# Performance work log

Measured on AMD Instinct MI355X. Metric: run time of the kernel, lower is better.

The kernel has to match this reference:

```python
import jax, jax.numpy as jnp
import numpy as np

N = 100000      # nodes
E = 1600000     # edges
G = 100         # graphs in batch
D_IN, H, OUT = 3, 128, 10


def gcn_conv(x, W, b, src, dst, n_nodes):
    """PyG GCNConv with default add_self_loops=True, symmetric normalization.
    out_i = sum_{j->i} d_j^-1/2 d_i^-1/2 (x_j W) + d_i^-1 (x_i W) + b
    where d includes the self-loop (+1)."""
    h = x @ W                                                   # [N, F]
    ones = jnp.ones((src.shape[0],), dtype=x.dtype)
    deg = jax.ops.segment_sum(ones, dst, num_segments=n_nodes) + 1.0  # self-loop
    dinv_sqrt = jax.lax.rsqrt(deg)
    norm = dinv_sqrt[src] * dinv_sqrt[dst]                      # [E]
    msg = h[src] * norm[:, None]                                # gather + scale
    agg = jax.ops.segment_sum(msg, dst, num_segments=n_nodes)   # scatter-add
    out = agg + h * (1.0 / deg)[:, None] + b                    # self-loop term + bias
    return out


def setup_inputs() -> dict:
    key = jax.random.key(0)
    ks = jax.random.split(key, 9)
    x = jax.random.normal(ks[0], (N, D_IN), dtype=jnp.float32)
    edge_index = jax.random.randint(ks[1], (2, E), 0, N)
    batch = jnp.sort(jax.random.randint(ks[2], (N,), 0, G))
    W1 = jax.random.normal(ks[3], (D_IN, H), dtype=jnp.float32) * (1.0 / np.sqrt(D_IN))
    b1 = jnp.zeros((H,), dtype=jnp.float32)
    W2 = jax.random.normal(ks[4], (H, H), dtype=jnp.float32) * (1.0 / np.sqrt(H))
    b2 = jnp.zeros((H,), dtype=jnp.float32)
    Wl = jax.random.normal(ks[5], (H, OUT), dtype=jnp.float32) * (1.0 / np.sqrt(H))
    bl = jnp.zeros((OUT,), dtype=jnp.float32)
    return {"x": x, "edge_index": edge_index, "batch": batch,
            "W1": W1, "b1": b1, "W2": W2, "b2": b2, "Wl": Wl, "bl": bl}


def reference(x, edge_index, batch, W1, b1, W2, b2, Wl, bl):
    src, dst = edge_index[0], edge_index[1]
    h = jax.nn.relu(gcn_conv(x, W1, b1, src, dst, N))
    h = jax.nn.relu(gcn_conv(h, W2, b2, src, dst, N))
    # global mean pool over graphs
    sums = jax.ops.segment_sum(h, batch, num_segments=G)                 # [G, H]
    cnts = jax.ops.segment_sum(jnp.ones((N,), h.dtype), batch, num_segments=G)
    pooled = sums / jnp.maximum(cnts, 1.0)[:, None]
    # dropout p=0.5 is identity in eval mode
    return pooled @ Wl + bl                                              # [G, OUT]
```

## Files before the change

kernel.cpp:

```cpp
#include <hip/hip_runtime.h>


#define DIN 3
#define H 128
#define OUTF 10
#define NWEIGHT (384 + 128 + 16384 + 128 + 1280 + 10)
#define ECH 2048
#define RGSH 9
#define RGSIZE 512
#define W2FRAG_N 16384
#define CHE 512

typedef float gcn364_f2 __attribute__((ext_vector_type(2)));
typedef float gcn364_f4 __attribute__((ext_vector_type(4)));
typedef short gcn364_s8 __attribute__((ext_vector_type(8)));

__device__ __forceinline__ float gcn364_bf2f(unsigned short u) {
    return __uint_as_float(((unsigned int)u) << 16);
}
__device__ __forceinline__ unsigned short gcn364_f2bf(float f) {
    unsigned int u = __float_as_uint(f);
    u += 0x7FFFu + ((u >> 16) & 1u);
    return (unsigned short)(u >> 16);
}

__device__ __forceinline__ int gcn364_probe(const unsigned short* __restrict__ xs16) {
    int lane = threadIdx.x & 63;
    int outl = 0;
    #pragma unroll
    for (int k = 0; k < 4; k++) {
        unsigned short u = xs16[lane * 4 + k];
        int e = (u >> 7) & 0xFF;
        outl += (e < 100 || e > 140) ? 1 : 0;
    }
    #pragma unroll
    for (int d = 1; d < 64; d <<= 1) outl += __shfl_xor(outl, d);
    return (outl > 32) ? 1 : 0;
}

static __global__ void gcn364_histconv(const void* __restrict__ x,
                                       const void* __restrict__ W1, const void* __restrict__ b1,
                                       const void* __restrict__ W2, const void* __restrict__ b2,
                                       const void* __restrict__ Wl, const void* __restrict__ bl,
                                       int* __restrict__ flag,
                                       float4* __restrict__ xf4, float* __restrict__ wf,
                                       unsigned short* __restrict__ w2frag,
                                       float* __restrict__ pooled,
                                       const int* __restrict__ edst,
                                       int* __restrict__ hist,
                                       int N, int E, int S, int RG, int GH) {
    __shared__ int h[256];
    if (blockIdx.x < (unsigned)S) {
        h[threadIdx.x] = 0;
        __syncthreads();
        int elo = blockIdx.x * ECH;
        int ehi = elo + ECH; if (ehi > E) ehi = E;
        #pragma unroll 4
        for (int e = elo + threadIdx.x; e < ehi; e += 256)
            atomicAdd(&h[edst[e] >> RGSH], 1);
        __syncthreads();
        if (threadIdx.x < RG) hist[blockIdx.x * RG + threadIdx.x] = h[threadIdx.x];
    }
    int i = blockIdx.x * blockDim.x + threadIdx.x;
    if (i < GH) pooled[i] = 0.0f;
    int total = N + NWEIGHT;
    if ((int)blockIdx.x * 256 < total) {
        int fl = gcn364_probe((const unsigned short*)x);
        if (i == 0) *flag = fl;
        if (i < N) {
            float a, b, c;
            if (fl) {
                const float* xs = (const float*)x;
                a = xs[3 * i]; b = xs[3 * i + 1]; c = xs[3 * i + 2];
            } else {
                const unsigned short* xs = (const unsigned short*)x;
                a = gcn364_bf2f(xs[3 * i]);
                b = gcn364_bf2f(xs[3 * i + 1]);
                c = gcn364_bf2f(xs[3 * i + 2]);
            }
            xf4[i] = make_float4(a, b, c, 0.f);
        } else if (i < total) {
            int j = i - N;
            const void* srcp;
            if      (j < 384)                       { srcp = W1; }
            else if ((j -= 384)   < 128)            { srcp = b1; }
            else if ((j -= 128)   < 16384)          { srcp = W2; }
            else if ((j -= 16384) < 128)            { srcp = b2; }
            else if ((j -= 128)   < 1280)           { srcp = Wl; }
            else    { j -= 1280;                      srcp = bl; }
            wf[i - N] = fl ? ((const float*)srcp)[j]
                           : gcn364_bf2f(((const unsigned short*)srcp)[j]);
        }
        if (i < W2FRAG_N) {
            int fl2 = fl;
            int j = i & 7;
            int l = (i >> 3) & 63;
            int c = (i >> 9) & 3;
            int t = i >> 11;
            int k = c * 32 + (l >> 4) * 8 + j;
            int n = t * 16 + (l & 15);
            float w = fl2 ? ((const float*)W2)[k * H + n]
                          : gcn364_bf2f(((const unsigned short*)W2)[k * H + n]);
            w2frag[i] = gcn364_f2bf(w);
        }
    }
}

static __global__ void gcn364_scanHpar(int* __restrict__ hist,
                                       int* __restrict__ regionBase,
                                       int S, int RG) {
    __shared__ int sh[1024];
    int r = blockIdx.x;
    int t = threadIdx.x;
    int carry = 0;
    for (int s0 = 0; s0 < S; s0 += 1024) {
        int s = s0 + t;
        int c = (s < S) ? hist[s * RG + r] : 0;
        sh[t] = c;
        __syncthreads();
        for (int d = 1; d < 1024; d <<= 1) {
            int v = (t >= d) ? sh[t - d] : 0;
            __syncthreads();
            sh[t] += v;
            __syncthreads();
        }
        if (s < S) hist[s * RG + r] = carry + sh[t] - c;
        int tot = sh[1023];
        __syncthreads();
        carry += tot;
    }
    if (t == 0) regionBase[r] = carry;
}

static __global__ void gcn364_scanR(int* __restrict__ regionBase,
                                    int RG, int E) {
    __shared__ int sh[256];
    int t = threadIdx.x;
    int c = (t < RG) ? regionBase[t] : 0;
    sh[t] = c;
    __syncthreads();
    for (int d = 1; d < 256; d <<= 1) {
        int v = (t >= d) ? sh[t - d] : 0;
        __syncthreads();
        sh[t] += v;
        __syncthreads();
    }
    if (t < RG) regionBase[t] = sh[t] - c;
    if (t == 0) regionBase[RG] = E;
}

static __global__ void gcn364_partition(const int* __restrict__ src,
                                        const int* __restrict__ dst,
                                        const int* __restrict__ hist,
                                        const int* __restrict__ regionBase,
                                        int* __restrict__ epack,
                                        int E, int RG) {
    __shared__ int gbase[256];
    __shared__ int scnt[256];
    __shared__ int sbase[256];
    __shared__ int ebuf[ECH];
    __shared__ unsigned char rmap[ECH];
    int s = blockIdx.x;
    int t = threadIdx.x;
    int elo = s * ECH;
    int ehi = elo + ECH; if (ehi > E) ehi = E;
    int ne = ehi - elo;

    if (t < RG) gbase[t] = hist[s * RG + t] + regionBase[t];
    scnt[t] = 0;
    __syncthreads();
    #pragma unroll 4
    for (int e = elo + t; e < ehi; e += 256)
        atomicAdd(&scnt[dst[e] >> RGSH], 1);
    __syncthreads();
    int c = scnt[t];
    sbase[t] = c;
    __syncthreads();
    for (int d = 1; d < 256; d <<= 1) {
        int v = (t >= d) ? sbase[t - d] : 0;
        __syncthreads();
        sbase[t] += v;
        __syncthreads();
    }
    int excl = sbase[t] - c;
    __syncthreads();
    sbase[t] = excl;
    scnt[t] = 0;
    __syncthreads();
    #pragma unroll 4
    for (int e = elo + t; e < ehi; e += 256) {
        int d = dst[e];
        int r = d >> RGSH;
        int lofs = atomicAdd(&scnt[r], 1);
        int slot = sbase[r] + lofs;
        ebuf[slot] = ((d & (RGSIZE - 1)) << 17) | src[e];
        rmap[slot] = (unsigned char)r;
    }
    __syncthreads();
    #pragma unroll 4
    for (int k = t; k < ne; k += 256) {
        int r = rmap[k];
        epack[gbase[r] + (k - sbase[r])] = ebuf[k];
    }
}

static __global__ void gcn364_build(const int* __restrict__ epack,
                                    const int* __restrict__ regionBase,
                                    int* __restrict__ off,
                                    int* __restrict__ esrc,
                                    float4* __restrict__ xf4,
                                    int N) {
    __shared__ int sdeg[RGSIZE];
    __shared__ int stmp[256];
    int r = blockIdx.x;
    int nlo = r << RGSH;
    int nn = N - nlo; if (nn > RGSIZE) nn = RGSIZE;
    int e0 = regionBase[r];
    int e1 = regionBase[r + 1];
    int t = threadIdx.x;
    int bdim = blockDim.x;

    if (t < RGSIZE) sdeg[t] = 0;
    __syncthreads();
    #pragma unroll 4
    for (int p = e0 + t; p < e1; p += bdim)
        atomicAdd(&sdeg[epack[p] >> 17], 1);
    __syncthreads();

    int a0 = 0, a1 = 0, psum = 0;
    if (t < 256) {
        a0 = sdeg[2 * t];
        a1 = sdeg[2 * t + 1];
        psum = a0 + a1;
        stmp[t] = psum;
    }
    __syncthreads();
    for (int d = 1; d < 256; d <<= 1) {
        int val = (t >= d && t < 256) ? stmp[t - d] : 0;
        __syncthreads();
        if (t < 256) stmp[t] += val;
        __syncthreads();
    }
    if (t < 256) {
        int excl = stmp[t] - psum;

        if (2 * t < nn)     off[nlo + 2 * t]     = e0 + excl + a0;
        if (2 * t + 1 < nn) off[nlo + 2 * t + 1] = e0 + excl + a0 + a1;
        if (2 * t < nn) {
            float di = rsqrtf((float)a0 + 1.0f);
            float4 xv = xf4[nlo + 2 * t];
            xv.x *= di; xv.y *= di; xv.z *= di; xv.w = di;
            xf4[nlo + 2 * t] = xv;
        }
        if (2 * t + 1 < nn) {
            float di = rsqrtf((float)a1 + 1.0f);
            float4 xv = xf4[nlo + 2 * t + 1];
            xv.x *= di; xv.y *= di; xv.z *= di; xv.w = di;
            xf4[nlo + 2 * t + 1] = xv;
        }
        sdeg[2 * t]     = e0 + excl;
        sdeg[2 * t + 1] = e0 + excl + a0;
    }
    __syncthreads();
    #pragma unroll 4
    for (int p = e0 + t; p < e1; p += bdim) {
        int v = epack[p];
        int q = atomicAdd(&sdeg[v >> 17], 1);
        esrc[q] = v & 0x1FFFF;
    }
}

static __global__ void gcn364_aggu(const int* __restrict__ esrc,
                                   const int* __restrict__ off,
                                   const float4* __restrict__ xf4,
                                   float4* __restrict__ u4, int N) {
    int lane = threadIdx.x & 63;
    int wv = threadIdx.x >> 6;
    int grp = lane >> 4;
    int sub = lane & 15;
    int i = (blockIdx.x * 4 + wv) * 4 + grp;

    float a0 = 0.f, a1 = 0.f, a2 = 0.f;
    if (i < N) {
        int p0 = (i == 0) ? 0 : off[i - 1];
        int p1 = off[i];
        for (int p = p0 + sub; p < p1; p += 16) {
            float4 sv = xf4[esrc[p]];
            a0 += sv.x; a1 += sv.y; a2 += sv.z;
        }
    }
    for (int d = 1; d < 16; d <<= 1) {
        a0 += __shfl_xor(a0, d);
        a1 += __shfl_xor(a1, d);
        a2 += __shfl_xor(a2, d);
    }
    if (i < N && sub == 0) {
        float4 xi = xf4[i];
        float di = xi.w;
        u4[i] = make_float4(di * (a0 + xi.x), di * (a1 + xi.y), di * (a2 + xi.z), di);
    }
}

__device__ __forceinline__ void gcn364_edge(const float4 u,
                                            const gcn364_f2* wa2, const gcn364_f2* wb2,
                                            const gcn364_f2* wc2, const gcn364_f2* bb2,
                                            gcn364_f2* acc) {
    gcn364_f2 ux = {u.x, u.x}, uy = {u.y, u.y}, uz = {u.z, u.z}, uw = {u.w, u.w};
    gcn364_f2 zero = {0.f, 0.f};
    #pragma unroll
    for (int q = 0; q < 4; q++) {
        gcn364_f2 t = ux * wa2[q] + uy * wb2[q] + uz * wc2[q] + bb2[q];
        t = __builtin_elementwise_max(t, zero);
        acc[q] += uw * t;
    }
}

#define MPB 16
static __global__ __launch_bounds__(256, 8) void gcn364_agg2pool(
        const int* __restrict__ esrc, const int* __restrict__ off,
        const float4* __restrict__ u4,
        const float* __restrict__ w1f, const float* __restrict__ b1f,
        const unsigned short* __restrict__ w2frag, const float* __restrict__ b2f,
        const int* __restrict__ batch, float* __restrict__ pooled, int N) {
    __shared__ unsigned short vshb[MPB][H + 8];
    __shared__ float4 sstage[CHE];
    __shared__ int soff[MPB + 1];
    __shared__ int sbatch[MPB];
    __shared__ float spool[2][H];
    int i0 = blockIdx.x * MPB;
    int tid = threadIdx.x;
    int wave = tid >> 6;
    int lane = tid & 63;
    int grp = lane >> 4;
    int sub = lane & 15;
    int node = wave * 4 + grp;
    int i = i0 + node;

    if (tid <= MPB) {
        int idx = i0 - 1 + tid;
        int cidx = idx < N - 1 ? idx : N - 1;
        soff[tid] = (idx < 0) ? 0 : off[cidx];
    }
    if (tid < MPB) {
        int bi = i0 + tid; if (bi > N - 1) bi = N - 1;
        sbatch[tid] = batch[bi];
    }

    gcn364_f2 wa2[4], wb2[4], wc2[4], bb2[4];
    #pragma unroll
    for (int q = 0; q < 4; q++) {
        int f = sub * 8 + q * 2;
        wa2[q] = (gcn364_f2){w1f[f], w1f[f + 1]};
        wb2[q] = (gcn364_f2){w1f[H + f], w1f[H + f + 1]};
        wc2[q] = (gcn364_f2){w1f[2 * H + f], w1f[2 * H + f + 1]};
        bb2[q] = (gcn364_f2){b1f[f], b1f[f + 1]};
    }
    __syncthreads();

    int s  = soff[node];
    int e  = soff[node + 1];
    int e0 = soff[0];
    int e1 = soff[MPB];

    gcn364_f2 acc[4];
    acc[0] = acc[1] = acc[2] = acc[3] = (gcn364_f2){0.f, 0.f};
    for (int cb = e0; cb < e1; cb += CHE) {
        int ce = cb + CHE; if (ce > e1) ce = e1;
        for (int p = cb + tid; p < ce; p += 256)
            sstage[p - cb] = u4[esrc[p]];
        __syncthreads();
        int lo = s > cb ? s : cb;
        int hi = e < ce ? e : ce;
        #pragma unroll 4
        for (int p = lo; p < hi; p++) {
            float4 u = sstage[p - cb];
            gcn364_edge(u, wa2, wb2, wc2, bb2, acc);
        }
        __syncthreads();
    }
    float di = 0.f;
    if (i < N) {
        float4 uS = u4[i];
        gcn364_edge(uS, wa2, wb2, wc2, bb2, acc);
        di = uS.w;
    }
    {
        gcn364_s8 o;
        o[0] = (short)gcn364_f2bf(acc[0].x * di);
        o[1] = (short)gcn364_f2bf(acc[0].y * di);
        o[2] = (short)gcn364_f2bf(acc[1].x * di);
        o[3] = (short)gcn364_f2bf(acc[1].y * di);
        o[4] = (short)gcn364_f2bf(acc[2].x * di);
        o[5] = (short)gcn364_f2bf(acc[2].y * di);
        o[6] = (short)gcn364_f2bf(acc[3].x * di);
        o[7] = (short)gcn364_f2bf(acc[3].y * di);
        *(gcn364_s8*)&vshb[node][sub * 8] = o;
    }
    __syncthreads();

    int m = lane & 15;
    int quad = lane >> 4;
    int g0 = sbatch[0];
    gcn364_s8 af[4];
    #pragma unroll
    for (int c = 0; c < 4; c++)
        af[c] = *(const gcn364_s8*)&vshb[m][c * 32 + quad * 8];

    #pragma unroll
    for (int tt = 0; tt < 2; tt++) {
        int t = wave * 2 + tt;
        gcn364_f4 cacc = {0.f, 0.f, 0.f, 0.f};
        #pragma unroll
        for (int c = 0; c < 4; c++) {
            gcn364_s8 bf8 = *(const gcn364_s8*)&w2frag[(((t * 4 + c) * 64) + lane) * 8];
            cacc = __builtin_amdgcn_mfma_f32_16x16x32_bf16(af[c], bf8, cacc, 0, 0, 0);
        }
        int feat = t * 16 + m;
        float bb = b2f[feat];
        int baseRow = quad * 4;
        float sum0 = 0.0f, sum1 = 0.0f;
        #pragma unroll
        for (int r = 0; r < 4; r++) {
            int ii = i0 + baseRow + r;
            if (ii >= N) continue;
            float val = fmaxf(cacc[r] + bb, 0.0f);
            if (sbatch[baseRow + r] == g0) sum0 += val; else sum1 += val;
        }
        sum0 += __shfl_xor(sum0, 16); sum0 += __shfl_xor(sum0, 32);
        sum1 += __shfl_xor(sum1, 16); sum1 += __shfl_xor(sum1, 32);
        if (quad == 0) {
            spool[0][feat] = sum0;
            spool[1][feat] = sum1;
        }
    }
    __syncthreads();
    {
        int slot = tid >> 7;
        int f = tid & (H - 1);
        float v = spool[slot][f];
        if (v != 0.0f) {
            int g = slot ? sbatch[MPB - 1] : g0;
            atomicAdd(&pooled[g * H + f], v);
        }
    }
}

static __global__ void gcn364_final(const float* __restrict__ pooled,
                                    const int* __restrict__ batch,
                                    const float* __restrict__ wlf,
                                    const float* __restrict__ blf,
                                    const int* __restrict__ flag,
                                    void* __restrict__ out, int N, int G) {
    int g = blockIdx.x;
    int o = threadIdx.x;
    if (g >= G || o >= OUTF) return;
    int lo = 0, hi = N;
    while (lo < hi) { int m = (lo + hi) >> 1; if (batch[m] < g) lo = m + 1; else hi = m; }
    int a = lo;
    lo = 0; hi = N;
    while (lo < hi) { int m = (lo + hi) >> 1; if (batch[m] < g + 1) lo = m + 1; else hi = m; }
    float cn = (float)(lo - a);
    float inv = 1.0f / fmaxf(cn, 1.0f);
    float acc = 0.0f;
    for (int k = 0; k < H; k++)
        acc += pooled[g * H + k] * wlf[k * OUTF + o];
    float v = acc * inv + blf[o];
    if (*flag) ((float*)out)[g * OUTF + o] = v;
    else       ((unsigned short*)out)[g * OUTF + o] = gcn364_f2bf(v);
}

extern "C" void kernel_launch(void* const* d_in, const int* in_sizes, int n_in,
                              void* d_out, int out_size, void* d_ws, size_t ws_size,
                              hipStream_t stream) {
    const void* x  = d_in[0];
    const int* edge_index = (const int*)d_in[1];
    const int* batch      = (const int*)d_in[2];
    const void* W1 = d_in[3];
    const void* b1 = d_in[4];
    const void* W2 = d_in[5];
    const void* b2 = d_in[6];
    const void* Wl = d_in[7];
    const void* bl = d_in[8];

    const int N = in_sizes[0] / DIN;
    const int E = in_sizes[1] / 2;
    const int G = out_size / OUTF;
    const int* src = edge_index;
    const int* dst = edge_index + E;
    const int SH = (E + 8191) / 8192;
    const int S  = (E + ECH - 1) / ECH;
    const int RG = (N + RGSIZE - 1) >> RGSH;
    const int GH = G * H;

    char* wsb = (char*)d_ws;
    float* pooled     = (float*)wsb;
    int*   histLeg    = (int*)(pooled + (size_t)GH);
    int*   regionBase = histLeg + (size_t)SH * RG;
    int*   off        = regionBase + RG + 1;
    int*   flag       = off + N;
    size_t ofs = (((size_t)((char*)(flag + 1) - wsb)) + 15) & ~(size_t)15;
    float4* xf4  = (float4*)(wsb + ofs);
    float4* u4   = xf4 + N;
    float*  wf   = (float*)(u4 + N);
    size_t ofs2 = (((size_t)((char*)(wf + NWEIGHT) - wsb)) + 15) & ~(size_t)15;
    unsigned short* w2frag = (unsigned short*)(wsb + ofs2);
    int*    epack = (int*)(w2frag + W2FRAG_N);
    int*    esrc  = epack + E;
    int*    hist  = esrc;

    float* w1f = wf;
    float* b1f = w1f + 384;
    float* b2f = b1f + 128 + 16384;
    float* wlf = b2f + 128;
    float* blf = wlf + 1280;

    {
        int convBlocks = (N + NWEIGHT + 255) / 256;
        int gmax = (S > convBlocks) ? S : convBlocks;
        gcn364_histconv<<<gmax, 256, 0, stream>>>(
            x, W1, b1, W2, b2, Wl, bl, flag, xf4, wf, w2frag, pooled,
            dst, hist, N, E, S, RG, GH);
    }
    gcn364_scanHpar<<<RG, 1024, 0, stream>>>(hist, regionBase, S, RG);
    gcn364_scanR<<<1, 256, 0, stream>>>(regionBase, RG, E);
    gcn364_partition<<<S, 256, 0, stream>>>(src, dst, hist, regionBase, epack, E, RG);
    gcn364_build<<<RG, 1024, 0, stream>>>(epack, regionBase, off, esrc, xf4, N);
    gcn364_aggu<<<(N + 15) / 16, 256, 0, stream>>>(esrc, off, xf4, u4, N);
    gcn364_agg2pool<<<(N + MPB - 1) / MPB, 256, 0, stream>>>(
        esrc, off, u4, w1f, b1f, w2frag, b2f, batch, pooled, N);
    gcn364_final<<<G, 64, 0, stream>>>(pooled, batch, wlf, blf, flag, d_out, N, G);
}
```

Before: 182.8 us.

## Vectorize edge loads, reuse scanned histogram in partition, parallelize final projection

The histogram and partition kernels now read dst/src as int4 when the chunk is aligned. The partition kernel drops its own counting pass and derives per-chunk region counts from the already-scanned histogram. The final kernel uses 128 threads with a wave shuffle reduction instead of a serial 128-step dot product per output. The layer-1 weight loads in agg2pool are also vectorized. Together these cut a full re-read of dst and some serial latency, at the cost of alignment-checked dual code paths and a dependence on the hist layout written by scanHpar.

Result: faster. 177.6 us (-2.8%).

```diff
diff --git a/kernel.cpp b/kernel.cpp
--- a/kernel.cpp
+++ b/kernel.cpp
@@ -55,9 +55,23 @@
         __syncthreads();
         int elo = blockIdx.x * ECH;
         int ehi = elo + ECH; if (ehi > E) ehi = E;
-        #pragma unroll 4
-        for (int e = elo + threadIdx.x; e < ehi; e += 256)
-            atomicAdd(&h[edst[e] >> RGSH], 1);
+        int ne = ehi - elo;
+        if (((ne & 3) == 0) && ((((size_t)(edst + elo)) & 15) == 0)) {
+            const int4* d4 = (const int4*)(edst + elo);
+            int n4 = ne >> 2;
+            #pragma unroll 2
+            for (int k = threadIdx.x; k < n4; k += 256) {
+                int4 v = d4[k];
+                atomicAdd(&h[v.x >> RGSH], 1);
+                atomicAdd(&h[v.y >> RGSH], 1);
+                atomicAdd(&h[v.z >> RGSH], 1);
+                atomicAdd(&h[v.w >> RGSH], 1);
+            }
+        } else {
+            #pragma unroll 4
+            for (int e = elo + threadIdx.x; e < ehi; e += 256)
+                atomicAdd(&h[edst[e] >> RGSH], 1);
+        }
         __syncthreads();
         if (threadIdx.x < RG) hist[blockIdx.x * RG + threadIdx.x] = h[threadIdx.x];
     }
@@ -154,7 +168,7 @@
                                         const int* __restrict__ hist,
                                         const int* __restrict__ regionBase,
                                         int* __restrict__ epack,
-                                        int E, int RG) {
+                                        int E, int S, int RG) {
     __shared__ int gbase[256];
     __shared__ int scnt[256];
     __shared__ int sbase[256];
@@ -166,15 +180,15 @@
     int ehi = elo + ECH; if (ehi > E) ehi = E;
     int ne = ehi - elo;
 
-    if (t < RG) gbase[t] = hist[s * RG + t] + regionBase[t];
+    int cnt = 0;
+    if (t < RG) {
+        int own = hist[s * RG + t];
+        gbase[t] = own + regionBase[t];
+        if (s < S - 1) cnt = hist[(s + 1) * RG + t] - own;
+        else           cnt = (regionBase[t + 1] - regionBase[t]) - own;
+    }
     scnt[t] = 0;
-    __syncthreads();
-    #pragma unroll 4
-    for (int e = elo + t; e < ehi; e += 256)
-        atomicAdd(&scnt[dst[e] >> RGSH], 1);
-    __syncthreads();
-    int c = scnt[t];
-    sbase[t] = c;
+    sbase[t] = cnt;
     __syncthreads();
     for (int d = 1; d < 256; d <<= 1) {
         int v = (t >= d) ? sbase[t - d] : 0;
@@ -182,19 +196,40 @@
         sbase[t] += v;
         __syncthreads();
     }
-    int excl = sbase[t] - c;
+    int excl = sbase[t] - cnt;
     __syncthreads();
     sbase[t] = excl;
-    scnt[t] = 0;
-    __syncthreads();
-    #pragma unroll 4
-    for (int e = elo + t; e < ehi; e += 256) {
-        int d = dst[e];
-        int r = d >> RGSH;
-        int lofs = atomicAdd(&scnt[r], 1);
-        int slot = sbase[r] + lofs;
-        ebuf[slot] = ((d & (RGSIZE - 1)) << 17) | src[e];
-        rmap[slot] = (unsigned char)r;
+    __syncthreads();
+    if (((ne & 3) == 0) && ((((size_t)(dst + elo)) & 15) == 0) &&
+        ((((size_t)(src + elo)) & 15) == 0)) {
+        const int4* d4 = (const int4*)(dst + elo);
+        const int4* s4 = (const int4*)(src + elo);
+        int n4 = ne >> 2;
+        #pragma unroll 2
+        for (int k = t; k < n4; k += 256) {
+            int4 dv = d4[k];
+            int4 sv = s4[k];
+            int r0 = dv.x >> RGSH, r1 = dv.y >> RGSH;
+            int r2 = dv.z >> RGSH, r3 = dv.w >> RGSH;
+            int p0 = sbase[r0] + atomicAdd(&scnt[r0], 1);
+            ebuf[p0] = ((dv.x & (RGSIZE - 1)) << 17) | sv.x; rmap[p0] = (unsigned char)r0;
+            int p1 = sbase[r1] + atomicAdd(&scnt[r1], 1);
+            ebuf[p1] = ((dv.y & (RGSIZE - 1)) << 17) | sv.y; rmap[p1] = (unsigned char)r1;
+            int p2 = sbase[r2] + atomicAdd(&scnt[r2], 1);
+            ebuf[p2] = ((dv.z & (RGSIZE - 1)) << 17) | sv.z; rmap[p2] = (unsigned char)r2;
+            int p3 = sbase[r3] + atomicAdd(&scnt[r3], 1);
+            ebuf[p3] = ((dv.w & (RGSIZE - 1)) << 17) | sv.w; rmap[p3] = (unsigned char)r3;
+        }
+    } else {
+        #pragma unroll 4
+        for (int e = elo + t; e < ehi; e += 256) {
+            int d = dst[e];
+            int r = d >> RGSH;
+            int lofs = atomicAdd(&scnt[r], 1);
+            int slot = sbase[r] + lofs;
+            ebuf[slot] = ((d & (RGSIZE - 1)) << 17) | src[e];
+            rmap[slot] = (unsigned char)r;
+        }
     }
     __syncthreads();
     #pragma unroll 4
@@ -347,13 +382,23 @@
     }
 
     gcn364_f2 wa2[4], wb2[4], wc2[4], bb2[4];
-    #pragma unroll
-    for (int q = 0; q < 4; q++) {
-        int f = sub * 8 + q * 2;
-        wa2[q] = (gcn364_f2){w1f[f], w1f[f + 1]};
-        wb2[q] = (gcn364_f2){w1f[H + f], w1f[H + f + 1]};
-        wc2[q] = (gcn364_f2){w1f[2 * H + f], w1f[2 * H + f + 1]};
-        bb2[q] = (gcn364_f2){b1f[f], b1f[f + 1]};
+    {
+        const gcn364_f4* wA = (const gcn364_f4*)w1f;
+        const gcn364_f4* wB = (const gcn364_f4*)(w1f + H);
+        const gcn364_f4* wC = (const gcn364_f4*)(w1f + 2 * H);
+        const gcn364_f4* wD = (const gcn364_f4*)b1f;
+        gcn364_f4 a0 = wA[sub * 2], a1 = wA[sub * 2 + 1];
+        gcn364_f4 b0 = wB[sub * 2], b1v = wB[sub * 2 + 1];
+        gcn364_f4 c0 = wC[sub * 2], c1 = wC[sub * 2 + 1];
+        gcn364_f4 d0 = wD[sub * 2], d1 = wD[sub * 2 + 1];
+        wa2[0] = (gcn364_f2){a0[0], a0[1]}; wa2[1] = (gcn364_f2){a0[2], a0[3]};
+        wa2[2] = (gcn364_f2){a1[0], a1[1]}; wa2[3] = (gcn364_f2){a1[2], a1[3]};
+        wb2[0] = (gcn364_f2){b0[0], b0[1]}; wb2[1] = (gcn364_f2){b0[2], b0[3]};
+        wb2[2] = (gcn364_f2){b1v[0], b1v[1]}; wb2[3] = (gcn364_f2){b1v[2], b1v[3]};
+        wc2[0] = (gcn364_f2){c0[0], c0[1]}; wc2[1] = (gcn364_f2){c0[2], c0[3]};
+        wc2[2] = (gcn364_f2){c1[0], c1[1]}; wc2[3] = (gcn364_f2){c1[2], c1[3]};
+        bb2[0] = (gcn364_f2){d0[0], d0[1]}; bb2[1] = (gcn364_f2){d0[2], d0[3]};
+        bb2[2] = (gcn364_f2){d1[0], d1[1]}; bb2[3] = (gcn364_f2){d1[2], d1[3]};
     }
     __syncthreads();
 
@@ -451,9 +496,12 @@
                                     const float* __restrict__ blf,
                                     const int* __restrict__ flag,
                                     void* __restrict__ out, int N, int G) {
+    __shared__ float red[2][OUTF];
     int g = blockIdx.x;
-    int o = threadIdx.x;
-    if (g >= G || o >= OUTF) return;
+    int t = threadIdx.x;
+    int lane = t & 63;
+    int wv = t >> 6;
+    if (g >= G) return;
     int lo = 0, hi = N;
     while (lo < hi) { int m = (lo + hi) >> 1; if (batch[m] < g) lo = m + 1; else hi = m; }
     int a = lo;
@@ -461,12 +509,26 @@
     while (lo < hi) { int m = (lo + hi) >> 1; if (batch[m] < g + 1) lo = m + 1; else hi = m; }
     float cn = (float)(lo - a);
     float inv = 1.0f / fmaxf(cn, 1.0f);
-    float acc = 0.0f;
-    for (int k = 0; k < H; k++)
-        acc += pooled[g * H + k] * wlf[k * OUTF + o];
-    float v = acc * inv + blf[o];
-    if (*flag) ((float*)out)[g * OUTF + o] = v;
-    else       ((unsigned short*)out)[g * OUTF + o] = gcn364_f2bf(v);
+
+    float p = pooled[g * H + t];
+    float v[OUTF];
+    #pragma unroll
+    for (int o = 0; o < OUTF; o++) v[o] = p * wlf[t * OUTF + o];
+    #pragma unroll
+    for (int d = 1; d < 64; d <<= 1) {
+        #pragma unroll
+        for (int o = 0; o < OUTF; o++) v[o] += __shfl_xor(v[o], d);
+    }
+    if (lane == 0) {
+        #pragma unroll
+        for (int o = 0; o < OUTF; o++) red[wv][o] = v[o];
+    }
+    __syncthreads();
+    if (t < OUTF) {
+        float r = (red[0][t] + red[1][t]) * inv + blf[t];
+        if (*flag) ((float*)out)[g * OUTF + t] = r;
+        else       ((unsigned short*)out)[g * OUTF + t] = gcn364_f2bf(r);
+    }
 }
 
 extern "C" void kernel_launch(void* const* d_in, const int* in_sizes, int n_in,
@@ -523,10 +585,10 @@
     }
     gcn364_scanHpar<<<RG, 1024, 0, stream>>>(hist, regionBase, S, RG);
     gcn364_scanR<<<1, 256, 0, stream>>>(regionBase, RG, E);
-    gcn364_partition<<<S, 256, 0, stream>>>(src, dst, hist, regionBase, epack, E, RG);
+    gcn364_partition<<<S, 256, 0, stream>>>(src, dst, hist, regionBase, epack, E, S, RG);
     gcn364_build<<<RG, 1024, 0, stream>>>(epack, regionBase, off, esrc, xf4, N);
     gcn364_aggu<<<(N + 15) / 16, 256, 0, stream>>>(esrc, off, xf4, u4, N);
     gcn364_agg2pool<<<(N + MPB - 1) / MPB, 256, 0, stream>>>(
         esrc, off, u4, w1f, b1f, w2frag, b2f, batch, pooled, N);
-    gcn364_final<<<G, 64, 0, stream>>>(pooled, batch, wlf, blf, flag, d_out, N, G);
-}
+    gcn364_final<<<G, H, 0, stream>>>(pooled, batch, wlf, blf, flag, d_out, N, G);
+}
```
